# Performance work log

Measured on AMD Instinct MI355X. Metric: run time of the kernel, lower is better.

The kernel has to match this reference:

```python
import jax, jax.numpy as jnp
import numpy as np

K = 10          # tagset_size (hardcoded default in CRF)
START_TAG = 8
STOP_TAG = 9
NEG = -10000.0  # value used by the torch code for impossible transitions


def setup_inputs() -> dict:
    key = jax.random.key(0)
    k1, k2, k3 = jax.random.split(key, 3)
    B, T = 4096, 700
    feats = jax.random.normal(k1, (B, T, K), dtype=jnp.float32)
    lengths = jax.random.randint(k2, (B,), 1, T + 1, dtype=jnp.int32)
    transitions = jax.random.normal(k3, (K, K), dtype=jnp.float32)
    # CRF.__init__: transitions[START_TAG, :] = -10000; transitions[:, STOP_TAG] = -10000
    transitions = transitions.at[START_TAG, :].set(NEG).at[:, STOP_TAG].set(NEG)
    return {"feats": feats, "lengths": lengths, "transitions": transitions}


def reference(feats, lengths, transitions):
    """CNN_CRF.forward (post-CNN): sequence-mask the features, then batched
    Viterbi decode (CRF._viterbi_decode_sequential) as a single lax.scan.
    Returns (path_scores [B], best_paths [B, T] int32, zero-padded past length)."""
    B, T, Kt = feats.shape
    mask = jnp.arange(T)[None, :] < lengths[:, None]          # [B, T]
    feats = feats * mask[..., None].astype(feats.dtype)       # cnn_features masking

    fv0 = jnp.full((B, Kt), NEG, dtype=feats.dtype).at[:, START_TAG].set(0.0)
    tag_ids = jnp.arange(Kt, dtype=jnp.int32)

    def step(fv, xs):
        feat_t, m_t = xs                                      # [B,K], [B]
        # next_tag_var[b, next, prev] = forward_var[b, prev] + transitions[next, prev]
        ntv = fv[:, None, :] + transitions[None, :, :]
        best = jnp.argmax(ntv, axis=2).astype(jnp.int32)      # [B, K] best prev per next
        vv = jnp.max(ntv, axis=2)                             # [B, K]
        fv_new = vv + feat_t                                  # emit added after max
        fv = jnp.where(m_t[:, None], fv_new, fv)              # freeze past length
        bp = jnp.where(m_t[:, None], best, tag_ids[None, :])  # identity bp past length
        return fv, bp

    fv, bps = jax.lax.scan(step, fv0, (jnp.swapaxes(feats, 0, 1), mask.T))  # bps: [T,B,K]

    terminal = fv + transitions[STOP_TAG][None, :]            # [B, K]
    path_scores = jnp.max(terminal, axis=1)                   # [B]
    last_tag = jnp.argmax(terminal, axis=1).astype(jnp.int32) # [B]

    b_idx = jnp.arange(B)

    def backtrace(tag, bp_t):
        out = tag                                             # tag at position t
        tag = bp_t[b_idx, tag]                                # tag at position t-1
        return tag, out

    _, path = jax.lax.scan(backtrace, last_tag, bps, reverse=True)  # [T, B]
    path = jnp.swapaxes(path, 0, 1)                           # [B, T]
    path = jnp.where(mask, path, 0)                           # zero padding past length
    return path_scores, path
```

## Files before the change

kernel.cpp:

```cpp
#include <hip/hip_runtime.h>
#include <stdint.h>

#define TAGS 10
#define START_TAG 8
#define STOP_TAG 9
#define NEGV (-10000.0f)

#define DPP_I(x, ctrl) __builtin_amdgcn_update_dpp(0, (x), (ctrl), 0xF, 0xF, true)

typedef int v4i __attribute__((ext_vector_type(4)));

__device__ __forceinline__ float maxf3(float a, float b, float c) {
    return fmaxf(fmaxf(a, b), c);
}

#define GLOADI(dst, base, OFF) \
    asm volatile("global_load_dword %0, %1, off offset:" #OFF \
                 : "=v"(dst) : "v"(base))
#define GLOADQ(dst, addr) \
    asm volatile("global_load_dwordx4 %0, %1, off" \
                 : "=v"(dst) : "v"((const void*)(addr)) : "memory")
#define GLOAD8(BUF, BASE) { \
    const float* gb_ = (BASE); \
    GLOADI(BUF[0], gb_, 0);   GLOADI(BUF[1], gb_, 40); \
    GLOADI(BUF[2], gb_, 80);  GLOADI(BUF[3], gb_, 120); \
    GLOADI(BUF[4], gb_, 160); GLOADI(BUF[5], gb_, 200); \
    GLOADI(BUF[6], gb_, 240); GLOADI(BUF[7], gb_, 280); }
#define GLOAD8X(BUF, FB, TB) { \
    GLOADI(BUF[0], (FB) + (size_t)min(max((TB) + 0, 0), T - 1) * TAGS, 0); \
    GLOADI(BUF[1], (FB) + (size_t)min(max((TB) + 1, 0), T - 1) * TAGS, 0); \
    GLOADI(BUF[2], (FB) + (size_t)min(max((TB) + 2, 0), T - 1) * TAGS, 0); \
    GLOADI(BUF[3], (FB) + (size_t)min(max((TB) + 3, 0), T - 1) * TAGS, 0); \
    GLOADI(BUF[4], (FB) + (size_t)min(max((TB) + 4, 0), T - 1) * TAGS, 0); \
    GLOADI(BUF[5], (FB) + (size_t)min(max((TB) + 5, 0), T - 1) * TAGS, 0); \
    GLOADI(BUF[6], (FB) + (size_t)min(max((TB) + 6, 0), T - 1) * TAGS, 0); \
    GLOADI(BUF[7], (FB) + (size_t)min(max((TB) + 7, 0), T - 1) * TAGS, 0); }
#define WAITP { asm volatile("s_waitcnt vmcnt(17)" ::: "memory"); \
                __builtin_amdgcn_sched_barrier(0); }
#define PINFENCE __builtin_amdgcn_sched_barrier(0);

__global__ __launch_bounds__(64, 1) void crf_fb_fwd(
    const float* __restrict__ feats,
    const int*   __restrict__ lengths,
    const float* __restrict__ trans,
    uint8_t*     __restrict__ bpA,
    uint8_t*     __restrict__ bpC,
    float*       __restrict__ fvAo,
    float*       __restrict__ hws,
    int B, int T, int H, int ABLK, int NCpad)
{
    const int lane = threadIdx.x & 63;
    const int grp  = lane >> 4;
    const int n    = lane & 15;
    const int m    = n & 7;
    const bool odd = (n & 1);

    int srcv[8];
    srcv[0] = n;
    srcv[1] = DPP_I(n, 0x121);  srcv[2] = DPP_I(n, 0x122);
    srcv[3] = DPP_I(n, 0x123);  srcv[4] = DPP_I(n, 0x124);
    srcv[5] = DPP_I(n, 0x125);  srcv[6] = DPP_I(n, 0x126);
    srcv[7] = DPP_I(n, 0x127);

    int rsrc[8];
#pragma unroll
    for (int r = 0; r < 8; ++r) rsrc[r] = (srcv[r] & 7) ^ 7;

    if ((int)blockIdx.x < ABLK) {
        const int b4   = blockIdx.x * 4;
        const int b    = min(b4 + grp, B - 1);
        const int len  = lengths[b];
        const int lenA = min(len, H);
        const int l0 = lengths[min(b4 + 0, B - 1)];
        const int l1 = lengths[min(b4 + 1, B - 1)];
        const int l2 = lengths[min(b4 + 2, B - 1)];
        const int l3 = lengths[min(b4 + 3, B - 1)];
        const int HA = min(max(max(l0, l1), max(l2, l3)), H);
        const int blocksA = H >> 3;

        float trowR[8];
#pragma unroll
        for (int r = 0; r < 8; ++r)
            trowR[r] = trans[m * TAGS + (srcv[r] & 7)];

        const float* fb = feats + (size_t)b * T * TAGS + m;
        uint8_t* bpa_l = bpA + (size_t)b * blocksA * 32 + ((n >> 1) & 3) * 8;
        const bool stl = (n < 8) && !odd;

        float fv = trans[m * TAGS + START_TAG] + fb[0];

#define KLEAF_A(r, ctrl) { \
        int rot_ = DPP_I(__float_as_int(fv), (ctrl)); \
        float lv_ = __int_as_float(rot_) + trowR[r]; \
        k##r = __int_as_float((__float_as_int(lv_) & ~7) | rsrc[r]); }

#define STEP_A(TI, FEAT, ACCST) { \
        const int t_ = (TI); \
        float k0, k1, k2, k3, k4, k5, k6, k7; \
        { float lv_ = fv + trowR[0]; \
          k0 = __int_as_float((__float_as_int(lv_) & ~7) | rsrc[0]); } \
        KLEAF_A(1, 0x121) KLEAF_A(2, 0x122) KLEAF_A(3, 0x123) \
        KLEAF_A(4, 0x124) KLEAF_A(5, 0x125) KLEAF_A(6, 0x126) \
        KLEAF_A(7, 0x127) \
        const float p1_ = maxf3(k0, k1, k2); \
        const float p2_ = maxf3(k3, k4, k5); \
        const float p3_ = maxf3(k6, k7, p1_); \
        const float mm_ = fmaxf(p2_, p3_); \
        const int idx_  = (__float_as_int(mm_) & 7) ^ 7; \
        const int pidx_ = DPP_I(idx_, 0xB1); \
        const uint32_t byte_ = (uint32_t)(odd ? (pidx_ | (idx_ << 4)) \
                                              : (idx_ | (pidx_ << 4))); \
        ACCST; \
        const float fvn_ = mm_ + (FEAT); \
        fv = ((unsigned)(t_ - 1) < (unsigned)(lenA - 1)) ? fvn_ : fv; }

#define PH_A(USE, LD, T0) { \
        GLOAD8(LD, fb + (size_t)min((T0) + 16, T - 8) * TAGS); \
        WAITP \
        uint32_t accl, acch; \
        STEP_A((T0) + 0, USE[0], accl = byte_) \
        STEP_A((T0) + 1, USE[1], accl |= byte_ << 8) \
        STEP_A((T0) + 2, USE[2], accl |= byte_ << 16) \
        STEP_A((T0) + 3, USE[3], accl |= byte_ << 24) \
        STEP_A((T0) + 4, USE[4], acch = byte_) \
        STEP_A((T0) + 5, USE[5], acch |= byte_ << 8) \
        STEP_A((T0) + 6, USE[6], acch |= byte_ << 16) \
        STEP_A((T0) + 7, USE[7], acch |= byte_ << 24) \
        if ((T0) < H) { \
            if (stl) *(uint2*)(bpa_l + (size_t)((T0) >> 3) * 32) \
                         = make_uint2(accl, acch); } }

        PINFENCE
        float xb[8], yb[8], zb[8];
        GLOAD8(xb, fb);
        GLOAD8(yb, fb + (size_t)min(8, T - 8) * TAGS);
        if (n < 8) *(volatile float*)(fvAo + (size_t)b * 8 + m) = 0.0f;

        for (int t0 = 0; t0 < HA; t0 += 24) {
            PH_A(xb, zb, t0)
            PH_A(yb, xb, t0 + 8)
            PH_A(zb, yb, t0 + 16)
        }
#undef KLEAF_A
#undef STEP_A
#undef PH_A

        if (n < 8)
            fvAo[(size_t)b * 8 + m] = fv;
    } else {
        const int c4   = (blockIdx.x - ABLK) * 4;
        const int b    = min(c4 + grp, B - 1);
        const int len  = lengths[b];
        const int lenm1 = len - 1;
        const int l0 = lengths[min(c4 + 0, B - 1)];
        const int l1 = lengths[min(c4 + 1, B - 1)];
        const int l2 = lengths[min(c4 + 2, B - 1)];
        const int l3 = lengths[min(c4 + 3, B - 1)];
        const int maxlen = max(max(l0, l1), max(l2, l3));

        const int ktop = (maxlen > H) ? min(NCpad - 1, (maxlen - H - 1) >> 3) : -1;
        const int k0 = ((ktop + 3) / 3) * 3 - 1;

        float trowC[8];
#pragma unroll
        for (int r = 0; r < 8; ++r)
            trowC[r] = trans[(srcv[r] & 7) * TAGS + m];

        float h = trans[STOP_TAG * TAGS + m];
        const float* fb = feats + (size_t)b * T * TAGS + m;
        uint8_t* bpc_l = bpC + (size_t)b * NCpad * 32 + ((n >> 1) & 3) * 8;
        const bool stl = (n < 8) && !odd;

#define KLEAF_C(r, ctrl) { \
        int rot_ = DPP_I(__float_as_int(e_), (ctrl)); \
        float lv_ = __int_as_float(rot_) + trowC[r]; \
        k##r = __int_as_float((__float_as_int(lv_) & ~7) | rsrc[r]); }

#define STEP_C(K, J, FEAT, ACCST) { \
        const int t_ = H - 1 + 8 * (K) + (J); \
        const float e_ = h + (FEAT); \
        float k0, k1, k2, k3, k4, k5, k6, k7; \
        { float lv_ = e_ + trowC[0]; \
          k0 = __int_as_float((__float_as_int(lv_) & ~7) | rsrc[0]); } \
        KLEAF_C(1, 0x121) KLEAF_C(2, 0x122) KLEAF_C(3, 0x123) \
        KLEAF_C(4, 0x124) KLEAF_C(5, 0x125) KLEAF_C(6, 0x126) \
        KLEAF_C(7, 0x127) \
        const float p1_ = maxf3(k0, k1, k2); \
        const float p2_ = maxf3(k3, k4, k5); \
        const float p3_ = maxf3(k6, k7, p1_); \
        const float mm_ = fmaxf(p2_, p3_); \
        const int idx_  = (__float_as_int(mm_) & 7) ^ 7; \
        const int pidx_ = DPP_I(idx_, 0xB1); \
        const uint32_t byte_ = (uint32_t)(odd ? (pidx_ | (idx_ << 4)) \
                                              : (idx_ | (pidx_ << 4))); \
        ACCST; \
        h = (t_ < lenm1) ? mm_ : h; }

#define PH_C(USE, LD, K) { \
        GLOAD8X(LD, fb, H + 8 * ((K) - 2)) \
        WAITP \
        uint32_t accl, acch; \
        STEP_C(K, 7, USE[7], acch = byte_ << 24) \
        STEP_C(K, 6, USE[6], acch |= byte_ << 16) \
        STEP_C(K, 5, USE[5], acch |= byte_ << 8) \
        STEP_C(K, 4, USE[4], acch |= byte_) \
        STEP_C(K, 3, USE[3], accl = byte_ << 24) \
        STEP_C(K, 2, USE[2], accl |= byte_ << 16) \
        STEP_C(K, 1, USE[1], accl |= byte_ << 8) \
        STEP_C(K, 0, USE[0], accl |= byte_) \
        if (stl) *(uint2*)(bpc_l + (size_t)(K) * 32) = make_uint2(accl, acch); }

        PINFENCE
        float xb[8], yb[8], zb[8];
        GLOAD8X(xb, fb, H + 8 * k0)
        GLOAD8X(yb, fb, H + 8 * (k0 - 1))
        if (n < 8) *(volatile float*)(hws + (size_t)b * 8 + m) = 0.0f;

        for (int k = k0; k >= 0; k -= 3) {
            PH_C(xb, zb, k)
            PH_C(yb, xb, k - 1)
            PH_C(zb, yb, k - 2)
        }
#undef KLEAF_C
#undef STEP_C
#undef PH_C

        if (n < 8)
            hws[(size_t)b * 8 + m] = h;
    }
}

#define CH_(QA, QB, J) { \
    const uint32_t sA_ = (tag & 2) ? (uint32_t)QA[2 + ((J) >> 2)] \
                                   : (uint32_t)QA[(J) >> 2]; \
    const uint32_t sB_ = (tag & 2) ? (uint32_t)QB[2 + ((J) >> 2)] \
                                   : (uint32_t)QB[(J) >> 2]; \
    const uint32_t sel_ = (tag & 4) ? sB_ : sA_; \
    chv_ = (int)((sel_ >> (8 * ((J) & 3) + 4 * (tag & 1))) & 7); }

#define AITER(K, QA, QB, VMC) { \
    asm volatile("s_waitcnt vmcnt(" #VMC ")" ::: "memory"); \
    __builtin_amdgcn_sched_barrier(0); \
    const int k_ = (K); \
    float bufv[8]; \
    _Pragma("unroll") \
    for (int u = 7; u >= 0; --u) { \
        const int t_ = 8 * k_ + u; \
        const bool act_ = t_ < lenA; \
        bufv[u] = act_ ? (float)tag : 0.0f; \
        int chv_; CH_(QA, QB, u) \
        tag = (act_ && t_ >= 1) ? chv_ : tag; \
    } \
    float4* o4_ = (float4*)(orow + 8 * k_); \
    o4_[0] = make_float4(bufv[0], bufv[1], bufv[2], bufv[3]); \
    o4_[1] = make_float4(bufv[4], bufv[5], bufv[6], bufv[7]); \
    const int kn_ = (k_ - 4 < 0) ? 0 : (k_ - 4); \
    GLOADQ(QA, ab8 + (size_t)kn_ * 32); \
    GLOADQ(QB, ab8 + (size_t)kn_ * 32 + 16); }

#define CITER(K, QA, QB, VMC) { \
    asm volatile("s_waitcnt vmcnt(" #VMC ")" ::: "memory"); \
    __builtin_amdgcn_sched_barrier(0); \
    const int k_ = (K); \
    float bufv[8]; \
    _Pragma("unroll") \
    for (int j = 0; j < 8; ++j) { \
        const int t_ = H - 1 + 8 * k_ + j; \
        const bool act_ = t_ < len - 1; \
        int chv_; CH_(QA, QB, j) \
        tag = act_ ? chv_ : tag; \
        bufv[j] = act_ ? (float)tag : 0.0f; \
    } \
    const int p0_ = H + 8 * k_; \
    if (p0_ + 7 < T) { \
        float4* o4_ = (float4*)(orow + p0_); \
        o4_[0] = make_float4(bufv[0], bufv[1], bufv[2], bufv[3]); \
        o4_[1] = make_float4(bufv[4], bufv[5], bufv[6], bufv[7]); \
    } else { \
        _Pragma("unroll") \
        for (int j = 0; j < 8; ++j) \
            if (p0_ + j < T) orow[p0_ + j] = bufv[j]; \
    } \
    const int kn_ = (k_ + 4 >= NCu) ? (NCu - 1) : (k_ + 4); \
    GLOADQ(QA, cb8 + (size_t)kn_ * 32); \
    GLOADQ(QB, cb8 + (size_t)kn_ * 32 + 16); }

__global__ __launch_bounds__(64, 1) void crf_fb_bt(
    const int*     __restrict__ lengths,
    const uint8_t* __restrict__ bpA,
    const uint8_t* __restrict__ bpC,
    const float*   __restrict__ fvA,
    const float*   __restrict__ hws,
    float*         __restrict__ out_scores,
    float*         __restrict__ out_path,
    int B, int T, int H, int NCpad)
{
    const int rb = (B + 63) >> 6;
    const bool roleA = ((int)blockIdx.x < rb);
    const int s = (roleA ? (int)blockIdx.x : (int)blockIdx.x - rb) * 64 + threadIdx.x;
    if (s >= B) return;
    const int len = lengths[s];
    const int blocksA = H >> 3;
    const int NCu = (T - H + 7) >> 3;

    float fa[8], hh[8];
    {
        const float4* f4 = (const float4*)(fvA + (size_t)s * 8);
        float4 a = f4[0], c = f4[1];
        fa[0]=a.x; fa[1]=a.y; fa[2]=a.z; fa[3]=a.w;
        fa[4]=c.x; fa[5]=c.y; fa[6]=c.z; fa[7]=c.w;
        const float4* h4 = (const float4*)(hws + (size_t)s * 8);
        float4 d = h4[0], e = h4[1];
        hh[0]=d.x; hh[1]=d.y; hh[2]=d.z; hh[3]=d.w;
        hh[4]=e.x; hh[5]=e.y; hh[6]=e.z; hh[7]=e.w;
    }
    float best = fa[0] + hh[0];
    int bstar = 0;
#pragma unroll
    for (int nn = 1; nn < 8; ++nn) {
        const float v = fa[nn] + hh[nn];
        if (v > best) { best = v; bstar = nn; }
    }

    float* orow = out_path + (size_t)s * T;
    int tag = bstar;
    v4i Q0a, Q0b, Q1a, Q1b, Q2a, Q2b, Q3a, Q3b;

    if (roleA) {
        const int lenA = min(len, H);
        const uint8_t* ab8 = bpA + (size_t)s * blocksA * 32;
        const int kt = blocksA - 1;
        GLOADQ(Q3a, ab8 + (size_t)kt * 32);       GLOADQ(Q3b, ab8 + (size_t)kt * 32 + 16);
        GLOADQ(Q2a, ab8 + (size_t)(kt - 1) * 32); GLOADQ(Q2b, ab8 + (size_t)(kt - 1) * 32 + 16);
        GLOADQ(Q1a, ab8 + (size_t)(kt - 2) * 32); GLOADQ(Q1b, ab8 + (size_t)(kt - 2) * 32 + 16);
        GLOADQ(Q0a, ab8 + (size_t)(kt - 3) * 32); GLOADQ(Q0b, ab8 + (size_t)(kt - 3) * 32 + 16);
        AITER(kt,     Q3a, Q3b, 6)
        AITER(kt - 1, Q2a, Q2b, 8)
        AITER(kt - 2, Q1a, Q1b, 10)
        AITER(kt - 3, Q0a, Q0b, 12)
        for (int k = kt - 4; k >= 3; k -= 4) {
            AITER(k,     Q3a, Q3b, 12)
            AITER(k - 1, Q2a, Q2b, 12)
            AITER(k - 2, Q1a, Q1b, 12)
            AITER(k - 3, Q0a, Q0b, 12)
        }
    } else {
        out_scores[s] = best;
        const uint8_t* cb8 = bpC + (size_t)s * NCpad * 32;
        GLOADQ(Q0a, cb8);                    GLOADQ(Q0b, cb8 + 16);
        GLOADQ(Q1a, cb8 + 32);               GLOADQ(Q1b, cb8 + 48);
        GLOADQ(Q2a, cb8 + 64);               GLOADQ(Q2b, cb8 + 80);
        GLOADQ(Q3a, cb8 + 96);               GLOADQ(Q3b, cb8 + 112);
        CITER(0, Q0a, Q0b, 6)
        CITER(1, Q1a, Q1b, 8)
        CITER(2, Q2a, Q2b, 10)
        CITER(3, Q3a, Q3b, 12)
        for (int k = 4; k + 3 < NCu; k += 4) {
            CITER(k,     Q0a, Q0b, 12)
            CITER(k + 1, Q1a, Q1b, 12)
            CITER(k + 2, Q2a, Q2b, 12)
            CITER(k + 3, Q3a, Q3b, 12)
        }
    }
}

__global__ __launch_bounds__(64, 1) void crf_fused_small(
    const float* __restrict__ feats,
    const int*   __restrict__ lengths,
    const float* __restrict__ trans,
    float*       __restrict__ out_scores,
    float*       __restrict__ out_path,
    uint8_t*     __restrict__ bp4,
    int B, int T)
{
    const int lane = threadIdx.x & 63;
    const int grp  = lane >> 4;
    const int n    = lane & 15;
    const int m    = n & 7;
    const bool odd = (n & 1);
    const int b4   = blockIdx.x * 4;
    const int b    = min(b4 + grp, B - 1);

    const int len = lengths[b];
    const int l0 = lengths[min(b4 + 0, B - 1)];
    const int l1 = lengths[min(b4 + 1, B - 1)];
    const int l2 = lengths[min(b4 + 2, B - 1)];
    const int l3 = lengths[min(b4 + 3, B - 1)];
    const int maxlen = max(max(l0, l1), max(l2, l3));

    int srcv[8];
    srcv[0] = n;
    srcv[1] = DPP_I(n, 0x121);  srcv[2] = DPP_I(n, 0x122);
    srcv[3] = DPP_I(n, 0x123);  srcv[4] = DPP_I(n, 0x124);
    srcv[5] = DPP_I(n, 0x125);  srcv[6] = DPP_I(n, 0x126);
    srcv[7] = DPP_I(n, 0x127);

    float trowR[8];
    int   rsrc[8];
#pragma unroll
    for (int r = 0; r < 8; ++r) {
        const int sq = srcv[r] & 7;
        trowR[r] = trans[m * TAGS + sq];
        rsrc[r]  = sq ^ 7;
    }

    const float* fb = feats + (size_t)b * T * TAGS + m;
    uint8_t* bpb = bp4 + (size_t)b * T * 4 + (n >> 1);
    const bool store_lane = (n < 8) && !odd;

    float fv = trans[m * TAGS + START_TAG] + fb[0];

#define KLEAF_S(r, ctrl) { \
        int rot_ = DPP_I(__float_as_int(fv), (ctrl)); \
        float lv_ = __int_as_float(rot_) + trowR[r]; \
        k##r = __int_as_float((__float_as_int(lv_) & ~7) | rsrc[r]); }

#define STEP_S(TI, FEAT) { \
        const int t_ = (TI); \
        float k0, k1, k2, k3, k4, k5, k6, k7; \
        { float lv_ = fv + trowR[0]; \
          k0 = __int_as_float((__float_as_int(lv_) & ~7) | rsrc[0]); } \
        KLEAF_S(1, 0x121) KLEAF_S(2, 0x122) KLEAF_S(3, 0x123) \
        KLEAF_S(4, 0x124) KLEAF_S(5, 0x125) KLEAF_S(6, 0x126) \
        KLEAF_S(7, 0x127) \
        const float p1_ = maxf3(k0, k1, k2); \
        const float p2_ = maxf3(k3, k4, k5); \
        const float p3_ = maxf3(k6, k7, p1_); \
        const float mm_ = fmaxf(p2_, p3_); \
        const int   idx_  = (__float_as_int(mm_) & 7) ^ 7; \
        const int   pidx_ = DPP_I(idx_, 0xB1); \
        const int   lo_   = odd ? pidx_ : idx_; \
        const int   hi_   = odd ? idx_ : pidx_; \
        const float fvn_  = mm_ + (FEAT); \
        fv = (t_ < len) ? fvn_ : fv; \
        if (t_ < T) { \
            if (store_lane) \
                bpb[(size_t)t_ * 4] = (uint8_t)(lo_ | (hi_ << 4)); \
        } }

    float fc[8], fn[8];
#pragma unroll
    for (int i = 0; i < 8; ++i)
        fc[i] = fb[(size_t)min(1 + i, T - 1) * TAGS];

    for (int t0 = 1; t0 < maxlen; t0 += 8) {
#pragma unroll
        for (int i = 0; i < 8; ++i)
            fn[i] = fb[(size_t)min(t0 + 8 + i, T - 1) * TAGS];

        STEP_S(t0 + 0, fc[0]) STEP_S(t0 + 1, fc[1])
        STEP_S(t0 + 2, fc[2]) STEP_S(t0 + 3, fc[3])
        STEP_S(t0 + 4, fc[4]) STEP_S(t0 + 5, fc[5])
        STEP_S(t0 + 6, fc[6]) STEP_S(t0 + 7, fc[7])

#pragma unroll
        for (int i = 0; i < 8; ++i) fc[i] = fn[i];
    }
#undef KLEAF_S
#undef STEP_S

    const float term = fv + trans[STOP_TAG * TAGS + m];
    float kk = __int_as_float((__float_as_int(term) & ~7) | (m ^ 7));
    kk = fmaxf(kk, __int_as_float(DPP_I(__float_as_int(kk), 0x124)));
    kk = fmaxf(kk, __int_as_float(DPP_I(__float_as_int(kk), 0x122)));
    kk = fmaxf(kk, __int_as_float(DPP_I(__float_as_int(kk), 0x121)));
    int tag = (__float_as_int(kk) & 7) ^ 7;

    if (n == 0)
        out_scores[b] = kk;

    __builtin_amdgcn_s_waitcnt(0);
    __builtin_amdgcn_sched_barrier(0);

    if (n == 0) {
        const uint32_t* rw = (const uint32_t*)(bp4 + (size_t)b * T * 4);
        float* orow = out_path + (size_t)b * T;
        const int NB = (T + 15) / 16;
        uint32_t wA[16], wB[16];

        auto loadblk = [&](int bi, uint32_t* w) {
            if (bi < 0) return;
#pragma unroll
            for (int j = 0; j < 4; ++j) {
                const int tb = min(bi * 16 + 4 * j, T - 4);
                *(uint4*)&w[4 * j] = *(const uint4*)&rw[tb];
            }
        };
        auto compblk = [&](int bi, uint32_t* w) {
            float buf[16];
#pragma unroll
            for (int u = 15; u >= 0; --u) {
                const int t = bi * 16 + u;
                if (t < T) {
                    const bool act = t < len;
                    buf[u] = act ? (float)tag : 0.0f;
                    if (act) tag = (int)((w[u] >> (4 * tag)) & 15);
                }
            }
#pragma unroll
            for (int j = 0; j < 16; j += 4) {
                const int t = bi * 16 + j;
                if (t + 3 < T)
                    *(float4*)(orow + t) = make_float4(buf[j], buf[j+1], buf[j+2], buf[j+3]);
            }
        };

        int bi = NB - 1;
        loadblk(bi, wA);
        loadblk(bi - 1, wB);
        for (; bi >= 0; bi -= 2) {
            compblk(bi, wA);
            loadblk(bi - 2, wA);
            if (bi - 1 >= 0) compblk(bi - 1, wB);
            loadblk(bi - 3, wB);
        }
    }
}

extern "C" void kernel_launch(void* const* d_in, const int* in_sizes, int n_in,
                              void* d_out, int out_size, void* d_ws, size_t ws_size,
                              hipStream_t stream)
{
    const float* feats   = (const float*)d_in[0];
    const int*   lengths = (const int*)d_in[1];
    const float* trans   = (const float*)d_in[2];
    const int B = in_sizes[1];
    const int T = in_sizes[0] / (B * TAGS);

    float* out_scores = (float*)d_out;
    float* out_path   = (float*)d_out + B;

    const int H = ((T / 2) + 15) & ~15;
    const int blocksA = H >> 3;
    const int NCu = (T - H + 7) >> 3;
    const int NCpad = ((NCu + 3) / 3) * 3;

    const size_t szA = (size_t)B * blocksA * 32;
    const size_t szC = (size_t)B * NCpad * 32;
    const size_t need = szA + szC + (size_t)B * 64;

    const bool ok = (H >= 32) && (T > H + 1) && ((T & 3) == 0) && ((B & 3) == 0)
                    && ((blocksA & 3) == 0) && ((NCu & 3) == 0)
                    && (blocksA >= 8) && (NCu >= 8) && (need <= ws_size);

    if (ok) {
        uint8_t* bpA  = (uint8_t*)d_ws;
        uint8_t* bpC  = bpA + szA;
        float*   fvAo = (float*)(bpC + szC);
        float*   hws  = fvAo + (size_t)B * 8;
        const int ABLK = B / 4;

        crf_fb_fwd<<<2 * ABLK, 64, 0, stream>>>(
            feats, lengths, trans, bpA, bpC, fvAo, hws, B, T, H, ABLK, NCpad);

        const int rb = (B + 63) >> 6;
        crf_fb_bt<<<2 * rb, 64, 0, stream>>>(
            lengths, bpA, bpC, fvAo, hws, out_scores, out_path, B, T, H, NCpad);
    } else {
        uint8_t* bp4 = (uint8_t*)d_ws;
        crf_fused_small<<<(B + 3) / 4, 64, 0, stream>>>(
            feats, lengths, trans, out_scores, out_path, bp4, B, T);
    }
}
```

Before: 74.14 us.

## Sort sequences by length so each wave groups similar lengths

```diff
diff --git a/kernel.cpp b/kernel.cpp
--- a/kernel.cpp
+++ b/kernel.cpp
@@ -39,10 +39,38 @@
                 __builtin_amdgcn_sched_barrier(0); }
 #define PINFENCE __builtin_amdgcn_sched_barrier(0);
 
+__global__ __launch_bounds__(1024) void crf_sort(
+    const int* __restrict__ lengths, int* __restrict__ ord, int B)
+{
+    __shared__ int hist[1024];
+    __shared__ int offs[1024];
+    const int tid = threadIdx.x;
+    hist[tid] = 0;
+    __syncthreads();
+    for (int i = tid; i < B; i += 1024)
+        atomicAdd(&hist[min(max(lengths[i], 0), 1023)], 1);
+    __syncthreads();
+    offs[tid] = hist[tid];
+    __syncthreads();
+    for (int off = 1; off < 1024; off <<= 1) {
+        int v = (tid >= off) ? offs[tid - off] : 0;
+        __syncthreads();
+        offs[tid] += v;
+        __syncthreads();
+    }
+    hist[tid] = offs[tid] - hist[tid];
+    __syncthreads();
+    for (int i = tid; i < B; i += 1024) {
+        const int p = atomicAdd(&hist[min(max(lengths[i], 0), 1023)], 1);
+        ord[p] = i;
+    }
+}
+
 __global__ __launch_bounds__(64, 1) void crf_fb_fwd(
     const float* __restrict__ feats,
     const int*   __restrict__ lengths,
     const float* __restrict__ trans,
+    const int*   __restrict__ ord,
     uint8_t*     __restrict__ bpA,
     uint8_t*     __restrict__ bpC,
     float*       __restrict__ fvAo,
@@ -68,13 +96,13 @@
 
     if ((int)blockIdx.x < ABLK) {
         const int b4   = blockIdx.x * 4;
-        const int b    = min(b4 + grp, B - 1);
+        const int b    = ord[b4 + grp];
         const int len  = lengths[b];
         const int lenA = min(len, H);
-        const int l0 = lengths[min(b4 + 0, B - 1)];
-        const int l1 = lengths[min(b4 + 1, B - 1)];
-        const int l2 = lengths[min(b4 + 2, B - 1)];
-        const int l3 = lengths[min(b4 + 3, B - 1)];
+        const int l0 = lengths[ord[b4 + 0]];
+        const int l1 = lengths[ord[b4 + 1]];
+        const int l2 = lengths[ord[b4 + 2]];
+        const int l3 = lengths[ord[b4 + 3]];
         const int HA = min(max(max(l0, l1), max(l2, l3)), H);
         const int blocksA = H >> 3;
 
@@ -148,14 +176,15 @@
         if (n < 8)
             fvAo[(size_t)b * 8 + m] = fv;
     } else {
-        const int c4   = (blockIdx.x - ABLK) * 4;
-        const int b    = min(c4 + grp, B - 1);
+        const int g    = blockIdx.x - ABLK;
+        const int c4   = (ABLK - 1 - g) * 4;
+        const int b    = ord[c4 + grp];
         const int len  = lengths[b];
         const int lenm1 = len - 1;
-        const int l0 = lengths[min(c4 + 0, B - 1)];
-        const int l1 = lengths[min(c4 + 1, B - 1)];
-        const int l2 = lengths[min(c4 + 2, B - 1)];
-        const int l3 = lengths[min(c4 + 3, B - 1)];
+        const int l0 = lengths[ord[c4 + 0]];
+        const int l1 = lengths[ord[c4 + 1]];
+        const int l2 = lengths[ord[c4 + 2]];
+        const int l3 = lengths[ord[c4 + 3]];
         const int maxlen = max(max(l0, l1), max(l2, l3));
 
         const int ktop = (maxlen > H) ? min(NCpad - 1, (maxlen - H - 1) >> 3) : -1;
@@ -537,7 +566,7 @@
 
     const size_t szA = (size_t)B * blocksA * 32;
     const size_t szC = (size_t)B * NCpad * 32;
-    const size_t need = szA + szC + (size_t)B * 64;
+    const size_t need = szA + szC + (size_t)B * 64 + (size_t)B * 4;
 
     const bool ok = (H >= 32) && (T > H + 1) && ((T & 3) == 0) && ((B & 3) == 0)
                     && ((blocksA & 3) == 0) && ((NCu & 3) == 0)
@@ -548,10 +577,13 @@
         uint8_t* bpC  = bpA + szA;
         float*   fvAo = (float*)(bpC + szC);
         float*   hws  = fvAo + (size_t)B * 8;
+        int*     ord  = (int*)(hws + (size_t)B * 8);
         const int ABLK = B / 4;
 
+        crf_sort<<<1, 1024, 0, stream>>>(lengths, ord, B);
+
         crf_fb_fwd<<<2 * ABLK, 64, 0, stream>>>(
-            feats, lengths, trans, bpA, bpC, fvAo, hws, B, T, H, ABLK, NCpad);
+            feats, lengths, trans, ord, bpA, bpC, fvAo, hws, B, T, H, ABLK, NCpad);
 
         const int rb = (B + 63) >> 6;
         crf_fb_bt<<<2 * rb, 64, 0, stream>>>(
```

Measured after the change: 68.40 us. 7.7% less time.
